# Kernel optimization log

Measured on AMD Instinct MI355X. Metric: run time of the kernel, lower is better.

The kernel has to match this reference:

```python
import jax, jax.numpy as jnp
import numpy as np

B, T, C, H = 4, 2048, 1024, 16
D = C // H

def setup_inputs() -> dict:
    key = jax.random.key(0)
    ks = jax.random.split(key, 9)
    s = 0.02
    return {
        "x": jax.random.normal(ks[0], (B, T, C), dtype=jnp.float32),
        "Wq": jax.random.normal(ks[1], (C, C), dtype=jnp.float32) * s,
        "bq": jnp.zeros((C,), dtype=jnp.float32),
        "Wk": jax.random.normal(ks[2], (C, C), dtype=jnp.float32) * s,
        "bk": jnp.zeros((C,), dtype=jnp.float32),
        "Wv": jax.random.normal(ks[3], (C, C), dtype=jnp.float32) * s,
        "bv": jnp.zeros((C,), dtype=jnp.float32),
        "Wo": jax.random.normal(ks[4], (C, C), dtype=jnp.float32) * s,
        "bo": jnp.zeros((C,), dtype=jnp.float32),
    }

def reference(x, Wq, bq, Wk, bk, Wv, bv, Wo, bo):
    # torch nn.Linear: y = x @ W.T + b
    q = x @ Wq.T + bq  # (B,T,C)
    k = x @ Wk.T + bk
    v = x @ Wv.T + bv
    # (B,H,T,D)
    q = q.reshape(B, T, H, D).transpose(0, 2, 1, 3)
    k = k.reshape(B, T, H, D).transpose(0, 2, 1, 3)
    v = v.reshape(B, T, H, D).transpose(0, 2, 1, 3)
    scale = 1.0 / jnp.sqrt(jnp.asarray(D, dtype=q.dtype))
    att = jnp.einsum("bhqd,bhkd->bhqk", q, k) * scale  # (B,H,T,T)
    causal = jnp.tril(jnp.ones((T, T), dtype=bool))
    att = jnp.where(causal[None, None], att, jnp.asarray(-jnp.inf, dtype=att.dtype))
    att = jax.nn.softmax(att, axis=-1)
    y = jnp.einsum("bhqk,bhkd->bhqd", att, v)  # (B,H,T,D)
    y = y.transpose(0, 2, 1, 3).reshape(B, T, C)
    return y @ Wo.T + bo
```

## Files before the change

kernel.cpp:

```cpp
#include <hip/hip_runtime.h>
#include <hip/hip_bf16.h>
#include <stdint.h>

typedef unsigned short u16;
typedef __bf16 bf16x8 __attribute__((ext_vector_type(8)));
typedef float f32x4 __attribute__((ext_vector_type(4)));
typedef float f32x16 __attribute__((ext_vector_type(16)));

#define NB 4
#define NT 2048
#define NC 1024
#define NH 16
#define ND 64
#define NM 8192
#define KVB 64

__device__ __forceinline__ u16 f2bf(float f) {
  union { float f; uint32_t u; } v; v.f = f;
  return (u16)((v.u + 0x7FFFu + ((v.u >> 16) & 1u)) >> 16);
}

__device__ __forceinline__ uint32_t pk2(float a, float b) {
  union { __hip_bfloat162 h; uint32_t u; } c;
  c.h = __float22bfloat162_rn(float2{a, b});
  return c.u;
}

__device__ __forceinline__ float fexp2(float x) {
#if __has_builtin(__builtin_amdgcn_exp2f)
  return __builtin_amdgcn_exp2f(x);
#else
  return exp2f(x);
#endif
}

__device__ __forceinline__ void g2l16(const void* g, void* l) {
  __builtin_amdgcn_global_load_lds((__attribute__((address_space(1))) const void*)g,
                                   (__attribute__((address_space(3))) void*)l,
                                   16, 0, 0);
}

__global__ __launch_bounds__(256) void cvt4(const float* __restrict__ in,
                                            u16* __restrict__ out, int n4) {
  int i = blockIdx.x * 256 + threadIdx.x;
  if (i >= n4) return;
  float4 v = ((const float4*)in)[i];
  ushort4 o;
  o.x = f2bf(v.x); o.y = f2bf(v.y); o.z = f2bf(v.z); o.w = f2bf(v.w);
  ((ushort4*)out)[i] = o;
}

__global__ __launch_bounds__(256) void cvtW(const float* __restrict__ w0,
                                            const float* __restrict__ w1,
                                            const float* __restrict__ w2,
                                            const float* __restrict__ w3,
                                            u16* o0, u16* o1, u16* o2, u16* o3) {
  const int y = blockIdx.y;
  const float* in = (y == 0) ? w0 : (y == 1) ? w1 : (y == 2) ? w2 : w3;
  u16* out = (y == 0) ? o0 : (y == 1) ? o1 : (y == 2) ? o2 : o3;
  int i = blockIdx.x * 256 + threadIdx.x;
  float4 v = ((const float4*)in)[i];
  ushort4 o;
  o.x = f2bf(v.x); o.y = f2bf(v.y); o.z = f2bf(v.z); o.w = f2bf(v.w);
  ((ushort4*)out)[i] = o;
}

template <int EPI>
__global__ __launch_bounds__(256, 4) void gemmR(
    const u16* __restrict__ A,
    const u16* __restrict__ W0, const u16* __restrict__ W1, const u16* __restrict__ W2,
    const float* __restrict__ b0, const float* __restrict__ b1, const float* __restrict__ b2,
    void* o0, void* o1, void* o2, int K) {
  const int z = blockIdx.z;
  const u16* Bw = (z == 0) ? W0 : ((z == 1) ? W1 : W2);
  const float* bias = (z == 0) ? b0 : ((z == 1) ? b1 : b2);
  void* outp = (z == 0) ? o0 : ((z == 1) ? o1 : o2);

  __shared__ __align__(16) char SB[32768];

  const int nbn = 8;
  const int lb = (blockIdx.x & 7) * (gridDim.x >> 3) + (blockIdx.x >> 3);
  const int m0 = (lb / nbn) << 7;
  const int n0 = (lb % nbn) << 7;
  const int t = threadIdx.x;
  const int wid = t >> 6, lane = t & 63;
  const int wm = wid >> 1, wn = wid & 1;
  const int lo = lane & 15, hi = lane >> 4;

  const int rr = t >> 3;
  const int sc = ((t & 7) ^ (rr & 7)) << 3;
  const u16* Asrc = A + (size_t)(m0 + rr) * K + sc;
  const u16* Bsrc = Bw + (size_t)(n0 + rr) * K + sc;

  f32x4 acc[4][4] = {};

  const int NTILES = K >> 6;

  for (int kt = 0; kt < NTILES; ++kt) {
#pragma unroll
    for (int j = 0; j < 4; ++j)
      g2l16(Asrc + (size_t)(j * 32) * K + kt * 64, SB + t * 16 + j * 4096);
#pragma unroll
    for (int j = 0; j < 4; ++j)
      g2l16(Bsrc + (size_t)(j * 32) * K + kt * 64, SB + 16384 + t * 16 + j * 4096);
    __syncthreads();

#pragma unroll
    for (int kh = 0; kh < 2; ++kh) {
      const int slot = (((kh << 2) | hi) ^ (lo & 7)) << 4;
      bf16x8 af[4], bfr[4];
#pragma unroll
      for (int f = 0; f < 4; ++f)
        af[f] = *(const bf16x8*)(SB + (wm * 64 + f * 16 + lo) * 128 + slot);
#pragma unroll
      for (int g = 0; g < 4; ++g)
        bfr[g] = *(const bf16x8*)(SB + 16384 + (wn * 64 + g * 16 + lo) * 128 + slot);
      __builtin_amdgcn_s_setprio(1);
#pragma unroll
      for (int f = 0; f < 4; ++f)
#pragma unroll
        for (int g = 0; g < 4; ++g)
          acc[f][g] = __builtin_amdgcn_mfma_f32_16x16x32_bf16(af[f], bfr[g],
                                                              acc[f][g], 0, 0, 0);
      __builtin_amdgcn_s_setprio(0);
    }
    __syncthreads();
  }

  const float scl = (EPI == 0 && z == 0) ? 0.125f * 1.44269504089f : 1.0f;
#pragma unroll
  for (int f = 0; f < 4; ++f) {
#pragma unroll
    for (int g = 0; g < 4; ++g) {
#pragma unroll
      for (int r = 0; r < 4; ++r) {
        const int rg = m0 + wm * 64 + f * 16 + hi * 4 + r;
        const int cg = n0 + wn * 64 + g * 16 + lo;
        const float v = (acc[f][g][r] + bias[cg]) * scl;
        if (EPI == 0) {
          const int bb = rg >> 11, tt = rg & (NT - 1);
          const int hh = cg >> 6, dd = cg & (ND - 1);
          size_t idx;
          if (z == 2)
            idx = ((size_t)(bb * NH + hh) * ND + dd) * NT + tt;
          else
            idx = ((size_t)(bb * NH + hh) * NT + tt) * ND + dd;
          ((u16*)outp)[idx] = f2bf(v);
        } else {
          ((float*)outp)[(size_t)rg * NC + cg] = v;
        }
      }
    }
  }
}

__global__ __launch_bounds__(512, 4) void flash5(const u16* __restrict__ Q,
                                                 const u16* __restrict__ Kg,
                                                 const u16* __restrict__ Vtg,
                                                 u16* __restrict__ Y) {
  __shared__ __align__(16) char LDS[65536];

  const int n = blockIdx.x;
  const int xcd = n & 7, slot = n >> 3;
  const int bh = (xcd << 3) | (slot >> 3);
  const int pt = slot & 7;
  const int qtB = 15 - pt;
  const int bb = bh >> 4, hh = bh & (NH - 1);
  const int tid = threadIdx.x;
  const int lane = tid & 63;
  const int grp = tid >> 8;
  const int ws4 = (tid >> 6) & 3;
  const int ql = lane & 31, h5 = lane >> 5;
  const int swz = (ql & 7) << 4;

  const u16* Qb = Q + (size_t)bh * NT * ND;
  const u16* Kb = Kg + (size_t)bh * NT * ND;
  const u16* Vb = Vtg + (size_t)bh * ND * NT;

  const int ntA = 2 * pt + 2;
  const int kvb1 = 15 - 2 * pt;
  const int q0wB = (qtB << 7) + (ws4 << 5);

  int q0w = grp ? q0wB : (pt << 7) + (ws4 << 5);
  int qg = q0w + ql;

  bf16x8 qf[4];
#pragma unroll
  for (int s = 0; s < 4; ++s)
    qf[s] = *(const bf16x8*)(Qb + (size_t)qg * ND + s * 16 + h5 * 8);

  f32x16 O0 = 0.f, O1 = 0.f;
  float lr = 0.f;

  const int tl = tid & 255;
  char* myL = LDS + (grp << 15);

  auto kvof = [&](int it) {
    return grp ? (kvb1 + it) : (it < ntA ? it : it - ntA);
  };

  auto STAGE = [&](int buf, int kv) {
#pragma unroll
    for (int p = 0; p < 2; ++p) {
      const int c = tl + (p << 8);
      const int row = c >> 3;
      const int so = ((c & 7) << 4) ^ ((row & 7) << 4);
      g2l16((const char*)(Kb + (size_t)((kv << 6) + row) * ND) + so,
            myL + (buf << 14) + c * 16);
      g2l16((const char*)(Vb + (size_t)row * NT + (kv << 6)) + so,
            myL + (buf << 14) + 8192 + c * 16);
    }
  };

  auto WRITEY = [&](const f32x16& A0, const f32x16& A1, float inv, int qgl) {
    u16* Yb = Y + ((size_t)bb * NT + qgl) * NC + hh * ND;
#pragma unroll
    for (int rq = 0; rq < 16; rq += 4) {
      const int dbase = 2 * rq + 4 * h5;
      uint2 w2;
      w2.x = pk2(A0[rq] * inv, A0[rq + 1] * inv);
      w2.y = pk2(A0[rq + 2] * inv, A0[rq + 3] * inv);
      *(uint2*)(Yb + dbase) = w2;
      w2.x = pk2(A1[rq] * inv, A1[rq + 1] * inv);
      w2.y = pk2(A1[rq + 2] * inv, A1[rq + 3] * inv);
      *(uint2*)(Yb + 32 + dbase) = w2;
    }
  };

  STAGE(0, kvof(0));
  __syncthreads();

  for (int it = 0; it < 17; ++it) {
    const int buf = it & 1;
    if (it < 16) STAGE(buf ^ 1, kvof(it + 1));

    if (!grp && it == ntA) {
      const float lt = lr + __shfl_xor(lr, 32, 64);
      WRITEY(O0, O1, 1.f / lt, qg);
      O0 = 0.f; O1 = 0.f; lr = 0.f;
      q0w = q0wB; qg = q0w + ql;
#pragma unroll
      for (int s = 0; s < 4; ++s)
        qf[s] = *(const bf16x8*)(Qb + (size_t)qg * ND + s * 16 + h5 * 8);
    }

    const int kv0 = kvof(it) << 6;
    const char* Kc = myL + (buf << 14);
    const char* Vc = Kc + 8192;

    f32x16 Sa0 = 0.f, Sa1 = 0.f;
    __builtin_amdgcn_s_setprio(1);
#pragma unroll
    for (int s = 0; s < 4; ++s) {
      bf16x8 kf0 = *(const bf16x8*)(Kc + ql * 128 + ((s * 32 + h5 * 16) ^ swz));
      bf16x8 kf1 = *(const bf16x8*)(Kc + (32 + ql) * 128 + ((s * 32 + h5 * 16) ^ swz));
      Sa0 = __builtin_amdgcn_mfma_f32_32x32x16_bf16(kf0, qf[s], Sa0, 0, 0, 0);
      Sa1 = __builtin_amdgcn_mfma_f32_32x32x16_bf16(kf1, qf[s], Sa1, 0, 0, 0);
    }
    __builtin_amdgcn_s_setprio(0);

    if (kv0 + 63 > q0w) {
#pragma unroll
      for (int r = 0; r < 16; ++r) {
        const int kvb = kv0 + (r & 3) + 8 * (r >> 2) + 4 * h5;
        if (kvb > qg) Sa0[r] = -3e38f;
        if (kvb + 32 > qg) Sa1[r] = -3e38f;
      }
    }

    float t0 = 0.f, t1 = 0.f, t2 = 0.f, t3 = 0.f;
#pragma unroll
    for (int r = 0; r < 16; r += 4) {
      const float a0 = fexp2(Sa0[r]),     a1 = fexp2(Sa0[r + 1]);
      const float a2 = fexp2(Sa0[r + 2]), a3 = fexp2(Sa0[r + 3]);
      const float b0 = fexp2(Sa1[r]),     b1 = fexp2(Sa1[r + 1]);
      const float b2 = fexp2(Sa1[r + 2]), b3 = fexp2(Sa1[r + 3]);
      Sa0[r] = a0; Sa0[r + 1] = a1; Sa0[r + 2] = a2; Sa0[r + 3] = a3;
      Sa1[r] = b0; Sa1[r + 1] = b1; Sa1[r + 2] = b2; Sa1[r + 3] = b3;
      t0 += a0 + b0; t1 += a1 + b1; t2 += a2 + b2; t3 += a3 + b3;
    }
    lr += (t0 + t1) + (t2 + t3);

    __builtin_amdgcn_s_setprio(1);
#pragma unroll
    for (int ks = 0; ks < 4; ++ks) {
      const int k0 = ks & 1;
      const f32x16& Sk = (ks < 2) ? Sa0 : Sa1;
      const uint32_t a0 = pk2(Sk[8 * k0],     Sk[8 * k0 + 1]);
      const uint32_t a1 = pk2(Sk[8 * k0 + 2], Sk[8 * k0 + 3]);
      const uint32_t b0 = pk2(Sk[8 * k0 + 4], Sk[8 * k0 + 5]);
      const uint32_t b1 = pk2(Sk[8 * k0 + 6], Sk[8 * k0 + 7]);
      const uint32_t c0 = h5 ? b0 : a0, c1 = h5 ? b1 : a1;
      const uint32_t d0 = h5 ? a0 : b0, d1 = h5 ? a1 : b1;
      const uint32_t x0 = __shfl_xor(d0, 32, 64);
      const uint32_t x1 = __shfl_xor(d1, 32, 64);
      union { uint32_t u[4]; bf16x8 v; } pf;
      pf.u[0] = h5 ? x0 : c0;
      pf.u[1] = h5 ? x1 : c1;
      pf.u[2] = h5 ? c0 : x0;
      pf.u[3] = h5 ? c1 : x1;
      bf16x8 vf0 = *(const bf16x8*)(Vc + ql * 128 + ((ks * 32 + h5 * 16) ^ swz));
      bf16x8 vf1 = *(const bf16x8*)(Vc + (32 + ql) * 128 + ((ks * 32 + h5 * 16) ^ swz));
      O0 = __builtin_amdgcn_mfma_f32_32x32x16_bf16(vf0, pf.v, O0, 0, 0, 0);
      O1 = __builtin_amdgcn_mfma_f32_32x32x16_bf16(vf1, pf.v, O1, 0, 0, 0);
    }
    __builtin_amdgcn_s_setprio(0);

    __syncthreads();
  }

  const int cslot = (ws4 << 6) + lane;
  char* cb = LDS + cslot * 136;
  if (!grp) {
#pragma unroll
    for (int j = 0; j < 8; ++j) {
      *(float2*)(cb + j * 8)      = float2{O0[2 * j], O0[2 * j + 1]};
      *(float2*)(cb + 64 + j * 8) = float2{O1[2 * j], O1[2 * j + 1]};
    }
    *(float*)(cb + 128) = lr;
  }
  __syncthreads();
  if (grp) {
#pragma unroll
    for (int j = 0; j < 8; ++j) {
      const float2 u = *(const float2*)(cb + j * 8);
      const float2 v = *(const float2*)(cb + 64 + j * 8);
      O0[2 * j] += u.x; O0[2 * j + 1] += u.y;
      O1[2 * j] += v.x; O1[2 * j + 1] += v.y;
    }
    lr += *(const float*)(cb + 128);
    const float lt = lr + __shfl_xor(lr, 32, 64);
    WRITEY(O0, O1, 1.f / lt, qg);
  }
}

extern "C" void kernel_launch(void* const* d_in, const int* in_sizes, int n_in,
                              void* d_out, int out_size, void* d_ws, size_t ws_size,
                              hipStream_t stream) {
  const float* x  = (const float*)d_in[0];
  const float* Wq = (const float*)d_in[1];
  const float* bq = (const float*)d_in[2];
  const float* Wk = (const float*)d_in[3];
  const float* bk = (const float*)d_in[4];
  const float* Wv = (const float*)d_in[5];
  const float* bv = (const float*)d_in[6];
  const float* Wo = (const float*)d_in[7];
  const float* bo = (const float*)d_in[8];

  const size_t SZ_X = (size_t)NM * NC * 2;
  const size_t SZ_W = (size_t)NC * NC * 2;
  char* ws = (char*)d_ws;
  u16* xb  = (u16*)ws;
  u16* wqb = (u16*)(ws + SZ_X);
  u16* wkb = (u16*)(ws + SZ_X + 1 * SZ_W);
  u16* wvb = (u16*)(ws + SZ_X + 2 * SZ_W);
  u16* wob = (u16*)(ws + SZ_X + 3 * SZ_W);
  u16* vb  = (u16*)(ws + SZ_X + 4 * SZ_W);
  u16* yb  = (u16*)(ws + 2 * SZ_X + 4 * SZ_W);
  u16* qb = (u16*)d_out;
  u16* kb = (u16*)((char*)d_out + SZ_X);

  if (ws_size < 3 * SZ_X + 4 * SZ_W) return;

  cvt4<<<dim3(NM * NC / 4 / 256), 256, 0, stream>>>(x, xb, NM * NC / 4);
  cvtW<<<dim3(NC * NC / 4 / 256, 4), 256, 0, stream>>>(Wq, Wk, Wv, Wo,
                                                       wqb, wkb, wvb, wob);

  gemmR<0><<<dim3(512, 1, 3), 256, 0, stream>>>(
      xb, wqb, wkb, wvb, bq, bk, bv, qb, kb, vb, NC);

  flash5<<<dim3(512), 512, 0, stream>>>(qb, kb, vb, yb);

  gemmR<1><<<dim3(512, 1, 1), 256, 0, stream>>>(
      yb, wob, wob, wob, bo, bo, bo, d_out, d_out, d_out, NC);
}
```

Measured before the change: 164.6 us.

## Fuse Q/K/V projections into one GEMM kernel sharing the A tile

Replaces the three-way grid-z QKV GEMM with one kernel where each block loads its x tile once and multiplies it against Wq, Wk and Wv tiles held together in a 64KB LDS buffer, accumulating three 128x128 outputs. This cuts redundant reads of x from global memory and the number of blocks from 1536 to 512. In exchange, per-thread accumulator registers triple and occupancy drops (launch bounds 2, 64KB LDS). The output-projection GEMM is simplified to a non-templated version.

```diff
diff --git a/kernel.cpp b/kernel.cpp
--- a/kernel.cpp
+++ b/kernel.cpp
@@ -65,23 +65,16 @@
   ((ushort4*)out)[i] = o;
 }
 
-template <int EPI>
-__global__ __launch_bounds__(256, 4) void gemmR(
+__global__ __launch_bounds__(256, 2) void gemmQKV(
     const u16* __restrict__ A,
-    const u16* __restrict__ W0, const u16* __restrict__ W1, const u16* __restrict__ W2,
-    const float* __restrict__ b0, const float* __restrict__ b1, const float* __restrict__ b2,
-    void* o0, void* o1, void* o2, int K) {
-  const int z = blockIdx.z;
-  const u16* Bw = (z == 0) ? W0 : ((z == 1) ? W1 : W2);
-  const float* bias = (z == 0) ? b0 : ((z == 1) ? b1 : b2);
-  void* outp = (z == 0) ? o0 : ((z == 1) ? o1 : o2);
-
-  __shared__ __align__(16) char SB[32768];
-
-  const int nbn = 8;
-  const int lb = (blockIdx.x & 7) * (gridDim.x >> 3) + (blockIdx.x >> 3);
-  const int m0 = (lb / nbn) << 7;
-  const int n0 = (lb % nbn) << 7;
+    const u16* __restrict__ Wq, const u16* __restrict__ Wk, const u16* __restrict__ Wv,
+    const float* __restrict__ bq, const float* __restrict__ bk, const float* __restrict__ bv,
+    u16* __restrict__ oq, u16* __restrict__ ok, u16* __restrict__ ov, int K) {
+  __shared__ __align__(16) char SB[65536];
+
+  const int lb = (blockIdx.x & 7) * 64 + (blockIdx.x >> 3);
+  const int m0 = (lb >> 3) << 7;
+  const int n0 = (lb & 7) << 7;
   const int t = threadIdx.x;
   const int wid = t >> 6, lane = t & 63;
   const int wm = wid >> 1, wn = wid & 1;
@@ -90,10 +83,98 @@
   const int rr = t >> 3;
   const int sc = ((t & 7) ^ (rr & 7)) << 3;
   const u16* Asrc = A + (size_t)(m0 + rr) * K + sc;
-  const u16* Bsrc = Bw + (size_t)(n0 + rr) * K + sc;
+  const u16* W0src = Wq + (size_t)(n0 + rr) * K + sc;
+  const u16* W1src = Wk + (size_t)(n0 + rr) * K + sc;
+  const u16* W2src = Wv + (size_t)(n0 + rr) * K + sc;
+
+  f32x4 acc[3][4][4] = {};
+
+  const int NTILES = K >> 6;
+
+  for (int kt = 0; kt < NTILES; ++kt) {
+#pragma unroll
+    for (int j = 0; j < 4; ++j) {
+      g2l16(Asrc + (size_t)(j * 32) * K + kt * 64, SB + t * 16 + j * 4096);
+      g2l16(W0src + (size_t)(j * 32) * K + kt * 64, SB + 16384 + t * 16 + j * 4096);
+      g2l16(W1src + (size_t)(j * 32) * K + kt * 64, SB + 32768 + t * 16 + j * 4096);
+      g2l16(W2src + (size_t)(j * 32) * K + kt * 64, SB + 49152 + t * 16 + j * 4096);
+    }
+    __syncthreads();
+
+#pragma unroll
+    for (int kh = 0; kh < 2; ++kh) {
+      const int slot = (((kh << 2) | hi) ^ (lo & 7)) << 4;
+      bf16x8 af[4];
+#pragma unroll
+      for (int f = 0; f < 4; ++f)
+        af[f] = *(const bf16x8*)(SB + (wm * 64 + f * 16 + lo) * 128 + slot);
+#pragma unroll
+      for (int w = 0; w < 3; ++w) {
+        bf16x8 bfr[4];
+#pragma unroll
+        for (int g = 0; g < 4; ++g)
+          bfr[g] = *(const bf16x8*)(SB + 16384 + w * 16384 +
+                                    (wn * 64 + g * 16 + lo) * 128 + slot);
+        __builtin_amdgcn_s_setprio(1);
+#pragma unroll
+        for (int f = 0; f < 4; ++f)
+#pragma unroll
+          for (int g = 0; g < 4; ++g)
+            acc[w][f][g] = __builtin_amdgcn_mfma_f32_16x16x32_bf16(af[f], bfr[g],
+                                                                   acc[w][f][g], 0, 0, 0);
+        __builtin_amdgcn_s_setprio(0);
+      }
+    }
+    __syncthreads();
+  }
+
+#pragma unroll
+  for (int w = 0; w < 3; ++w) {
+    u16* outp = (w == 0) ? oq : (w == 1) ? ok : ov;
+    const float* bias = (w == 0) ? bq : (w == 1) ? bk : bv;
+    const float scl = (w == 0) ? 0.125f * 1.44269504089f : 1.0f;
+#pragma unroll
+    for (int f = 0; f < 4; ++f) {
+#pragma unroll
+      for (int g = 0; g < 4; ++g) {
+#pragma unroll
+        for (int r = 0; r < 4; ++r) {
+          const int rg = m0 + wm * 64 + f * 16 + hi * 4 + r;
+          const int cg = n0 + wn * 64 + g * 16 + lo;
+          const float v = (acc[w][f][g][r] + bias[cg]) * scl;
+          const int bb = rg >> 11, tt = rg & (NT - 1);
+          const int hh = cg >> 6, dd = cg & (ND - 1);
+          size_t idx;
+          if (w == 2)
+            idx = ((size_t)(bb * NH + hh) * ND + dd) * NT + tt;
+          else
+            idx = ((size_t)(bb * NH + hh) * NT + tt) * ND + dd;
+          outp[idx] = f2bf(v);
+        }
+      }
+    }
+  }
+}
+
+__global__ __launch_bounds__(256, 4) void gemmR(
+    const u16* __restrict__ A, const u16* __restrict__ W0,
+    const float* __restrict__ b0, float* __restrict__ outp, int K) {
+  __shared__ __align__(16) char SB[32768];
+
+  const int lb = (blockIdx.x & 7) * (gridDim.x >> 3) + (blockIdx.x >> 3);
+  const int m0 = (lb / 8) << 7;
+  const int n0 = (lb % 8) << 7;
+  const int t = threadIdx.x;
+  const int wid = t >> 6, lane = t & 63;
+  const int wm = wid >> 1, wn = wid & 1;
+  const int lo = lane & 15, hi = lane >> 4;
+
+  const int rr = t >> 3;
+  const int sc = ((t & 7) ^ (rr & 7)) << 3;
+  const u16* Asrc = A + (size_t)(m0 + rr) * K + sc;
+  const u16* Bsrc = W0 + (size_t)(n0 + rr) * K + sc;
 
   f32x4 acc[4][4] = {};
-
   const int NTILES = K >> 6;
 
   for (int kt = 0; kt < NTILES; ++kt) {
@@ -127,31 +208,16 @@
     __syncthreads();
   }
 
-  const float scl = (EPI == 0 && z == 0) ? 0.125f * 1.44269504089f : 1.0f;
-#pragma unroll
-  for (int f = 0; f < 4; ++f) {
-#pragma unroll
-    for (int g = 0; g < 4; ++g) {
+#pragma unroll
+  for (int f = 0; f < 4; ++f)
+#pragma unroll
+    for (int g = 0; g < 4; ++g)
 #pragma unroll
       for (int r = 0; r < 4; ++r) {
         const int rg = m0 + wm * 64 + f * 16 + hi * 4 + r;
         const int cg = n0 + wn * 64 + g * 16 + lo;
-        const float v = (acc[f][g][r] + bias[cg]) * scl;
-        if (EPI == 0) {
-          const int bb = rg >> 11, tt = rg & (NT - 1);
-          const int hh = cg >> 6, dd = cg & (ND - 1);
-          size_t idx;
-          if (z == 2)
-            idx = ((size_t)(bb * NH + hh) * ND + dd) * NT + tt;
-          else
-            idx = ((size_t)(bb * NH + hh) * NT + tt) * ND + dd;
-          ((u16*)outp)[idx] = f2bf(v);
-        } else {
-          ((float*)outp)[(size_t)rg * NC + cg] = v;
-        }
+        outp[(size_t)rg * NC + cg] = acc[f][g][r] + b0[cg];
       }
-    }
-  }
 }
 
 __global__ __launch_bounds__(512, 4) void flash5(const u16* __restrict__ Q,
@@ -366,11 +432,10 @@
   cvtW<<<dim3(NC * NC / 4 / 256, 4), 256, 0, stream>>>(Wq, Wk, Wv, Wo,
                                                        wqb, wkb, wvb, wob);
 
-  gemmR<0><<<dim3(512, 1, 3), 256, 0, stream>>>(
+  gemmQKV<<<dim3(512), 256, 0, stream>>>(
       xb, wqb, wkb, wvb, bq, bk, bv, qb, kb, vb, NC);
 
   flash5<<<dim3(512), 512, 0, stream>>>(qb, kb, vb, yb);
 
-  gemmR<1><<<dim3(512, 1, 1), 256, 0, stream>>>(
-      yb, wob, wob, wob, bo, bo, bo, d_out, d_out, d_out, NC);
-}
+  gemmR<<<dim3(512), 256, 0, stream>>>(yb, wob, bo, (float*)d_out, NC);
+}
```

Result: no change. 163.2 us (-0.9%).
